# Kernel optimization log

Measured on AMD Instinct MI355X. Metric: run time of the kernel, lower is better.

The kernel has to match this reference:

```python
import jax, jax.numpy as jnp
import numpy as np

BETA = 0.1       # reputation weight
GAMMA = 0.1      # load penalty weight
EXPL_C = 0.1     # UCB exploration constant
LOAD_EMA = 0.9   # load EMA alpha
TOP_K = 2
EPS = 1e-10


def setup_inputs() -> dict:
    key = jax.random.key(0)
    k1, k2, k3, k4, k5 = jax.random.split(key, 5)
    B, S, H, E = 4, 4096, 2048, 64
    return {
        "x": jax.random.normal(k1, (B, S, H), dtype=jnp.float32),
        "gate_w": jax.random.normal(k2, (E, H), dtype=jnp.float32) * (1.0 / np.sqrt(H)),
        "reputation": jax.random.normal(k3, (E,), dtype=jnp.float32),
        "loads": jax.random.uniform(k4, (E,), dtype=jnp.float32),
        "counts": jax.random.uniform(k5, (E,), dtype=jnp.float32),
        "total_decisions": 1000000,
    }


def reference(x, gate_w, reputation, loads, counts, total_decisions):
    B, S, H = x.shape
    E = gate_w.shape[0]
    x_flat = x.reshape(-1, H)                                  # [T, H]
    base_logits = jnp.einsum("th,eh->te", x_flat, gate_w)      # [T, E]

    # current_batch_assignments is None -> current_loads = expert_loads
    updated_loads = LOAD_EMA * loads + (1.0 - LOAD_EMA) * loads  # [E]

    # UCB-style exploration bonus, broadcast over tokens
    expl = EXPL_C * jnp.sqrt(jnp.log(jnp.float32(total_decisions) + 1.0) / (counts + EPS))  # [E]

    selection_scores = (base_logits
                        + BETA * reputation[None, :]
                        - GAMMA * updated_loads[None, :]
                        + expl[None, :])                        # [T, E]

    top_k_scores, top_k_indices = jax.lax.top_k(selection_scores, TOP_K)  # [T, K]
    routing_weights = jax.nn.softmax(top_k_scores, axis=-1).reshape(B, S, TOP_K)
    expert_indices = top_k_indices.reshape(B, S, TOP_K)

    # differentiable load-balancing aux loss
    router_probs = jax.nn.softmax(selection_scores.astype(jnp.float32), axis=-1)  # [T, E]
    expert_gate = jax.nn.one_hot(top_k_indices, E, dtype=jnp.float32).sum(axis=1)  # [T, E]
    tokens_per_expert = expert_gate.mean(axis=0)               # [E]
    router_prob_per_expert = router_probs.mean(axis=0)         # [E]
    aux_loss = (tokens_per_expert * router_prob_per_expert).sum() * E

    return routing_weights, expert_indices, aux_loss
```

## Files before the change

kernel.cpp:

```cpp
#include <hip/hip_runtime.h>
#include <cmath>

#define HDIM 2048
#define NEXP 64
#define TTOT 16384
#define BM   64
#define BK   32
#define NITER (HDIM / BK)
#define LDA  (BM + 4)
#define LDB  (NEXP + 4)
#define LDS_SC (NEXP + 4)

__global__ __launch_bounds__(256) void router_main(
    const float* __restrict__ x,
    const float* __restrict__ gw,
    const float* __restrict__ rep,
    const float* __restrict__ loads,
    const float* __restrict__ counts,
    const int*   __restrict__ total_dec,
    float* __restrict__ out_w,
    float* __restrict__ out_idx,
    float* __restrict__ prob_acc,
    float* __restrict__ gate_acc)
{
    __shared__ float a_s[2][BK][LDA];
    __shared__ float b_s[2][BK][LDB];
    __shared__ float sc_s[BM][LDS_SC];
    __shared__ float bias_s[NEXP];
    __shared__ float m_s[BM], z_s[BM];
    __shared__ int   i1_s[BM], i2_s[BM];

    const int tid = threadIdx.x;
    const int tx  = tid & 15;
    const int ty  = tid >> 4;
    const int r0  = tid >> 3;
    const int c4  = tid & 7;
    const int t0  = blockIdx.x * BM;

    if (tid < NEXP) {
        float L = logf((float)(*total_dec) + 1.0f);
        bias_s[tid] = 0.1f * rep[tid] - 0.1f * loads[tid]
                    + 0.1f * sqrtf(L / (counts[tid] + 1e-10f));
    }

    const int H4 = HDIM / 4;
    const float4* __restrict__ x4 = reinterpret_cast<const float4*>(x) + (size_t)t0 * H4;
    const float4* __restrict__ g4 = reinterpret_cast<const float4*>(gw);

    float acc[4][4] = {};

#define STORE_TILE(BUFI, A0, A1, B0, B1) do {                                  \
        float _t0[4] = {(A0).x, (A0).y, (A0).z, (A0).w};                       \
        float _t1[4] = {(A1).x, (A1).y, (A1).z, (A1).w};                       \
        float _t2[4] = {(B0).x, (B0).y, (B0).z, (B0).w};                       \
        float _t3[4] = {(B1).x, (B1).y, (B1).z, (B1).w};                       \
        _Pragma("unroll")                                                      \
        for (int u = 0; u < 4; ++u) {                                          \
            a_s[BUFI][c4 * 4 + u][r0]      = _t0[u];                           \
            a_s[BUFI][c4 * 4 + u][r0 + 32] = _t1[u];                           \
            b_s[BUFI][c4 * 4 + u][r0]      = _t2[u];                           \
            b_s[BUFI][c4 * 4 + u][r0 + 32] = _t3[u];                           \
        } } while (0)

    {
        float4 a0 = x4[(size_t)r0 * H4 + c4];
        float4 a1 = x4[(size_t)(r0 + 32) * H4 + c4];
        float4 b0 = g4[(size_t)r0 * H4 + c4];
        float4 b1 = g4[(size_t)(r0 + 32) * H4 + c4];
        STORE_TILE(0, a0, a1, b0, b1);
    }
    __syncthreads();

    int buf = 0;
    for (int it = 0; it < NITER; ++it) {
        float4 na0, na1, nb0, nb1;
        const bool has_next = (it + 1 < NITER);
        if (has_next) {
            const int k4 = (it + 1) * (BK / 4);
            na0 = x4[(size_t)r0 * H4 + k4 + c4];
            na1 = x4[(size_t)(r0 + 32) * H4 + k4 + c4];
            nb0 = g4[(size_t)r0 * H4 + k4 + c4];
            nb1 = g4[(size_t)(r0 + 32) * H4 + k4 + c4];
        }

        #pragma unroll
        for (int kk = 0; kk < BK; ++kk) {
            const float4 afv = *reinterpret_cast<const float4*>(&a_s[buf][kk][ty * 4]);
            const float4 bfv = *reinterpret_cast<const float4*>(&b_s[buf][kk][tx * 4]);
            const float af[4] = {afv.x, afv.y, afv.z, afv.w};
            const float bf[4] = {bfv.x, bfv.y, bfv.z, bfv.w};
            #pragma unroll
            for (int i = 0; i < 4; ++i)
                #pragma unroll
                for (int j = 0; j < 4; ++j)
                    acc[i][j] = fmaf(af[i], bf[j], acc[i][j]);
        }

        if (has_next) STORE_TILE(buf ^ 1, na0, na1, nb0, nb1);
        __syncthreads();
        buf ^= 1;
    }
#undef STORE_TILE

    #pragma unroll
    for (int i = 0; i < 4; ++i)
        #pragma unroll
        for (int j = 0; j < 4; ++j)
            sc_s[ty * 4 + i][tx * 4 + j] = acc[i][j] + bias_s[tx * 4 + j];
    __syncthreads();

    if (tid < BM) {
        const int t = tid;
        float m1 = -INFINITY, m2 = -INFINITY;
        int   i1 = 0, i2 = 0;
        for (int e = 0; e < NEXP; ++e) {
            const float s = sc_s[t][e];
            if (s > m1)      { m2 = m1; i2 = i1; m1 = s; i1 = e; }
            else if (s > m2) { m2 = s; i2 = e; }
        }
        float z = 0.0f;
        for (int e = 0; e < NEXP; ++e) z += expf(sc_s[t][e] - m1);

        const float e2  = expf(m2 - m1);
        const float inv = 1.0f / (1.0f + e2);
        const int   gt  = t0 + t;
        reinterpret_cast<float2*>(out_w)[gt]   = make_float2(inv, e2 * inv);
        reinterpret_cast<float2*>(out_idx)[gt] = make_float2((float)i1, (float)i2);
        m_s[t] = m1; z_s[t] = z; i1_s[t] = i1; i2_s[t] = i2;
    }
    __syncthreads();

    if (tid < NEXP) {
        const int e = tid;
        float ps = 0.0f, gs = 0.0f;
        for (int t = 0; t < BM; ++t) {
            ps += expf(sc_s[t][e] - m_s[t]) / z_s[t];
            gs += (float)((i1_s[t] == e) + (i2_s[t] == e));
        }
        atomicAdd(&prob_acc[e], ps);
        atomicAdd(&gate_acc[e], gs);
    }
}

__global__ void router_aux(const float* __restrict__ prob_acc,
                           const float* __restrict__ gate_acc,
                           float* __restrict__ out_aux)
{
    const float invT = 1.0f / (float)TTOT;
    const int e = threadIdx.x;
    float v = (gate_acc[e] * invT) * (prob_acc[e] * invT);
    #pragma unroll
    for (int off = 32; off > 0; off >>= 1)
        v += __shfl_down(v, off);
    if (e == 0) out_aux[0] = v * (float)NEXP;
}

extern "C" void kernel_launch(void* const* d_in, const int* in_sizes, int n_in,
                              void* d_out, int out_size, void* d_ws, size_t ws_size,
                              hipStream_t stream)
{
    const float* x      = (const float*)d_in[0];
    const float* gw     = (const float*)d_in[1];
    const float* rep    = (const float*)d_in[2];
    const float* loads  = (const float*)d_in[3];
    const float* counts = (const float*)d_in[4];
    const int*   total  = (const int*)d_in[5];

    float* out     = (float*)d_out;
    float* out_w   = out;
    float* out_idx = out + 32768;
    float* out_aux = out + 65536;

    float* prob_acc = (float*)d_ws;
    float* gate_acc = prob_acc + NEXP;

    hipMemsetAsync(d_ws, 0, 2 * NEXP * sizeof(float), stream);
    router_main<<<dim3(TTOT / BM), dim3(256), 0, stream>>>(
        x, gw, rep, loads, counts, total, out_w, out_idx, prob_acc, gate_acc);
    router_aux<<<dim3(1), dim3(64), 0, stream>>>(prob_acc, gate_acc, out_aux);
}
```

Before: 265.4 us.

## Split router GEMM along K into four partial blocks plus reduce kernel

The token-by-expert GEMM is split along the hidden dimension into four independent blocks per token tile, each writing partial logits to workspace. A separate reduce kernel sums the partials, adds the bias, and performs the top-2, softmax and aux accumulation. This quadruples the grid so that more waves are resident per CU and the one-block-per-CU latency bottleneck is reduced. In exchange it adds a partial-sum round trip through global memory and an extra launch, and it falls back to the fused kernel if the workspace is too small.

New measurement: 246.0 us. 1.08x faster.

```diff
diff --git a/kernel.cpp b/kernel.cpp
--- a/kernel.cpp
+++ b/kernel.cpp
@@ -2,50 +2,41 @@
 #include <cmath>
 
 #define HDIM 2048
+#define H4   (HDIM / 4)
 #define NEXP 64
 #define TTOT 16384
 #define BM   64
 #define BK   32
-#define NITER (HDIM / BK)
+#define NITER_FULL (HDIM / BK)
+#define KSPLIT 4
+#define NITER_K (NITER_FULL / KSPLIT)
 #define LDA  (BM + 4)
 #define LDB  (NEXP + 4)
-#define LDS_SC (NEXP + 4)
-
-__global__ __launch_bounds__(256) void router_main(
+#define LDS_SC 65
+
+#define WS_PARTIAL_OFF 128
+#define PARTIAL_FLOATS ((size_t)(TTOT / BM) * KSPLIT * BM * NEXP)
+
+__global__ __launch_bounds__(256, 4) void router_gemm_k(
     const float* __restrict__ x,
     const float* __restrict__ gw,
-    const float* __restrict__ rep,
-    const float* __restrict__ loads,
-    const float* __restrict__ counts,
-    const int*   __restrict__ total_dec,
-    float* __restrict__ out_w,
-    float* __restrict__ out_idx,
-    float* __restrict__ prob_acc,
-    float* __restrict__ gate_acc)
+    float* __restrict__ partial)
 {
     __shared__ float a_s[2][BK][LDA];
     __shared__ float b_s[2][BK][LDB];
-    __shared__ float sc_s[BM][LDS_SC];
-    __shared__ float bias_s[NEXP];
-    __shared__ float m_s[BM], z_s[BM];
-    __shared__ int   i1_s[BM], i2_s[BM];
 
     const int tid = threadIdx.x;
     const int tx  = tid & 15;
     const int ty  = tid >> 4;
     const int r0  = tid >> 3;
     const int c4  = tid & 7;
-    const int t0  = blockIdx.x * BM;
-
-    if (tid < NEXP) {
-        float L = logf((float)(*total_dec) + 1.0f);
-        bias_s[tid] = 0.1f * rep[tid] - 0.1f * loads[tid]
-                    + 0.1f * sqrtf(L / (counts[tid] + 1e-10f));
-    }
-
-    const int H4 = HDIM / 4;
-    const float4* __restrict__ x4 = reinterpret_cast<const float4*>(x) + (size_t)t0 * H4;
-    const float4* __restrict__ g4 = reinterpret_cast<const float4*>(gw);
+    const int tb  = blockIdx.x;
+    const int kg  = blockIdx.y;
+    const int t0  = tb * BM;
+    const int kb  = kg * (H4 / KSPLIT);
+
+    const float4* __restrict__ x4 = reinterpret_cast<const float4*>(x) + (size_t)t0 * H4 + kb;
+    const float4* __restrict__ g4 = reinterpret_cast<const float4*>(gw) + kb;
 
     float acc[4][4] = {};
 
@@ -72,9 +63,9 @@
     __syncthreads();
 
     int buf = 0;
-    for (int it = 0; it < NITER; ++it) {
+    for (int it = 0; it < NITER_K; ++it) {
         float4 na0, na1, nb0, nb1;
-        const bool has_next = (it + 1 < NITER);
+        const bool has_next = (it + 1 < NITER_K);
         if (has_next) {
             const int k4 = (it + 1) * (BK / 4);
             na0 = x4[(size_t)r0 * H4 + k4 + c4];
@@ -102,11 +93,47 @@
     }
 #undef STORE_TILE
 
+    float4* pout = reinterpret_cast<float4*>(partial + ((size_t)tb * KSPLIT + kg) * (BM * NEXP));
     #pragma unroll
     for (int i = 0; i < 4; ++i)
-        #pragma unroll
-        for (int j = 0; j < 4; ++j)
-            sc_s[ty * 4 + i][tx * 4 + j] = acc[i][j] + bias_s[tx * 4 + j];
+        pout[(ty * 4 + i) * (NEXP / 4) + tx] =
+            make_float4(acc[i][0], acc[i][1], acc[i][2], acc[i][3]);
+}
+
+__global__ __launch_bounds__(256) void router_reduce(
+    const float* __restrict__ partial,
+    const float* __restrict__ rep,
+    const float* __restrict__ loads,
+    const float* __restrict__ counts,
+    const int*   __restrict__ total_dec,
+    float* __restrict__ out_w,
+    float* __restrict__ out_idx,
+    float* __restrict__ prob_acc,
+    float* __restrict__ gate_acc)
+{
+    __shared__ float sc_s[BM][LDS_SC];
+    __shared__ float bias_s[NEXP];
+    __shared__ float m_s[BM], z_s[BM];
+    __shared__ int   i1_s[BM], i2_s[BM];
+
+    const int tid = threadIdx.x;
+    const int tb  = blockIdx.x;
+    const int t0  = tb * BM;
+
+    if (tid < NEXP) {
+        float L = logf((float)(*total_dec) + 1.0f);
+        bias_s[tid] = 0.1f * rep[tid] - 0.1f * loads[tid]
+                    + 0.1f * sqrtf(L / (counts[tid] + 1e-10f));
+    }
+    __syncthreads();
+
+    const float* p = partial + (size_t)tb * KSPLIT * (BM * NEXP);
+    #pragma unroll
+    for (int o = 0; o < (BM * NEXP) / 256; ++o) {
+        const int idx = o * 256 + tid;
+        float s = p[idx] + p[BM * NEXP + idx] + p[2 * BM * NEXP + idx] + p[3 * BM * NEXP + idx];
+        sc_s[idx >> 6][idx & 63] = s + bias_s[idx & 63];
+    }
     __syncthreads();
 
     if (tid < BM) {
@@ -142,6 +169,133 @@
     }
 }
 
+__global__ __launch_bounds__(256) void router_main(
+    const float* __restrict__ x,
+    const float* __restrict__ gw,
+    const float* __restrict__ rep,
+    const float* __restrict__ loads,
+    const float* __restrict__ counts,
+    const int*   __restrict__ total_dec,
+    float* __restrict__ out_w,
+    float* __restrict__ out_idx,
+    float* __restrict__ prob_acc,
+    float* __restrict__ gate_acc)
+{
+    __shared__ float a_s[2][BK][LDA];
+    __shared__ float b_s[2][BK][LDB];
+    __shared__ float sc_s[BM][LDS_SC];
+    __shared__ float bias_s[NEXP];
+    __shared__ float m_s[BM], z_s[BM];
+    __shared__ int   i1_s[BM], i2_s[BM];
+
+    const int tid = threadIdx.x;
+    const int tx  = tid & 15;
+    const int ty  = tid >> 4;
+    const int r0  = tid >> 3;
+    const int c4  = tid & 7;
+    const int t0  = blockIdx.x * BM;
+
+    if (tid < NEXP) {
+        float L = logf((float)(*total_dec) + 1.0f);
+        bias_s[tid] = 0.1f * rep[tid] - 0.1f * loads[tid]
+                    + 0.1f * sqrtf(L / (counts[tid] + 1e-10f));
+    }
+
+    const float4* __restrict__ x4 = reinterpret_cast<const float4*>(x) + (size_t)t0 * H4;
+    const float4* __restrict__ g4 = reinterpret_cast<const float4*>(gw);
+
+    float acc[4][4] = {};
+
+#define STORE_TILE(BUFI, A0, A1, B0, B1) do {                                  \
+        float _t0[4] = {(A0).x, (A0).y, (A0).z, (A0).w};                       \
+        float _t1[4] = {(A1).x, (A1).y, (A1).z, (A1).w};                       \
+        float _t2[4] = {(B0).x, (B0).y, (B0).z, (B0).w};                       \
+        float _t3[4] = {(B1).x, (B1).y, (B1).z, (B1).w};                       \
+        _Pragma("unroll")                                                      \
+        for (int u = 0; u < 4; ++u) {                                          \
+            a_s[BUFI][c4 * 4 + u][r0]      = _t0[u];                           \
+            a_s[BUFI][c4 * 4 + u][r0 + 32] = _t1[u];                           \
+            b_s[BUFI][c4 * 4 + u][r0]      = _t2[u];                           \
+            b_s[BUFI][c4 * 4 + u][r0 + 32] = _t3[u];                           \
+        } } while (0)
+
+    {
+        float4 a0 = x4[(size_t)r0 * H4 + c4];
+        float4 a1 = x4[(size_t)(r0 + 32) * H4 + c4];
+        float4 b0 = g4[(size_t)r0 * H4 + c4];
+        float4 b1 = g4[(size_t)(r0 + 32) * H4 + c4];
+        STORE_TILE(0, a0, a1, b0, b1);
+    }
+    __syncthreads();
+
+    int buf = 0;
+    for (int it = 0; it < NITER_FULL; ++it) {
+        float4 na0, na1, nb0, nb1;
+        const bool has_next = (it + 1 < NITER_FULL);
+        if (has_next) {
+            const int k4 = (it + 1) * (BK / 4);
+            na0 = x4[(size_t)r0 * H4 + k4 + c4];
+            na1 = x4[(size_t)(r0 + 32) * H4 + k4 + c4];
+            nb0 = g4[(size_t)r0 * H4 + k4 + c4];
+            nb1 = g4[(size_t)(r0 + 32) * H4 + k4 + c4];
+        }
+        #pragma unroll
+        for (int kk = 0; kk < BK; ++kk) {
+            const float4 afv = *reinterpret_cast<const float4*>(&a_s[buf][kk][ty * 4]);
+            const float4 bfv = *reinterpret_cast<const float4*>(&b_s[buf][kk][tx * 4]);
+            const float af[4] = {afv.x, afv.y, afv.z, afv.w};
+            const float bf[4] = {bfv.x, bfv.y, bfv.z, bfv.w};
+            #pragma unroll
+            for (int i = 0; i < 4; ++i)
+                #pragma unroll
+                for (int j = 0; j < 4; ++j)
+                    acc[i][j] = fmaf(af[i], bf[j], acc[i][j]);
+        }
+        if (has_next) STORE_TILE(buf ^ 1, na0, na1, nb0, nb1);
+        __syncthreads();
+        buf ^= 1;
+    }
+#undef STORE_TILE
+
+    #pragma unroll
+    for (int i = 0; i < 4; ++i)
+        #pragma unroll
+        for (int j = 0; j < 4; ++j)
+            sc_s[ty * 4 + i][tx * 4 + j] = acc[i][j] + bias_s[tx * 4 + j];
+    __syncthreads();
+
+    if (tid < BM) {
+        const int t = tid;
+        float m1 = -INFINITY, m2 = -INFINITY;
+        int   i1 = 0, i2 = 0;
+        for (int e = 0; e < NEXP; ++e) {
+            const float s = sc_s[t][e];
+            if (s > m1)      { m2 = m1; i2 = i1; m1 = s; i1 = e; }
+            else if (s > m2) { m2 = s; i2 = e; }
+        }
+        float z = 0.0f;
+        for (int e = 0; e < NEXP; ++e) z += expf(sc_s[t][e] - m1);
+        const float e2  = expf(m2 - m1);
+        const float inv = 1.0f / (1.0f + e2);
+        const int   gt  = t0 + t;
+        reinterpret_cast<float2*>(out_w)[gt]   = make_float2(inv, e2 * inv);
+        reinterpret_cast<float2*>(out_idx)[gt] = make_float2((float)i1, (float)i2);
+        m_s[t] = m1; z_s[t] = z; i1_s[t] = i1; i2_s[t] = i2;
+    }
+    __syncthreads();
+
+    if (tid < NEXP) {
+        const int e = tid;
+        float ps = 0.0f, gs = 0.0f;
+        for (int t = 0; t < BM; ++t) {
+            ps += expf(sc_s[t][e] - m_s[t]) / z_s[t];
+            gs += (float)((i1_s[t] == e) + (i2_s[t] == e));
+        }
+        atomicAdd(&prob_acc[e], ps);
+        atomicAdd(&gate_acc[e], gs);
+    }
+}
+
 __global__ void router_aux(const float* __restrict__ prob_acc,
                            const float* __restrict__ gate_acc,
                            float* __restrict__ out_aux)
@@ -173,9 +327,19 @@
 
     float* prob_acc = (float*)d_ws;
     float* gate_acc = prob_acc + NEXP;
-
-    hipMemsetAsync(d_ws, 0, 2 * NEXP * sizeof(float), stream);
-    router_main<<<dim3(TTOT / BM), dim3(256), 0, stream>>>(
-        x, gw, rep, loads, counts, total, out_w, out_idx, prob_acc, gate_acc);
+    float* partial  = (float*)d_ws + WS_PARTIAL_OFF;
+
+    const size_t ws_needed = (WS_PARTIAL_OFF + PARTIAL_FLOATS) * sizeof(float);
+
+    hipMemsetAsync(d_ws, 0, WS_PARTIAL_OFF * sizeof(float), stream);
+
+    if (ws_size >= ws_needed) {
+        router_gemm_k<<<dim3(TTOT / BM, KSPLIT), dim3(256), 0, stream>>>(x, gw, partial);
+        router_reduce<<<dim3(TTOT / BM), dim3(256), 0, stream>>>(
+            partial, rep, loads, counts, total, out_w, out_idx, prob_acc, gate_acc);
+    } else {
+        router_main<<<dim3(TTOT / BM), dim3(256), 0, stream>>>(
+            x, gw, rep, loads, counts, total, out_w, out_idx, prob_acc, gate_acc);
+    }
     router_aux<<<dim3(1), dim3(64), 0, stream>>>(prob_acc, gate_acc, out_aux);
 }
```
